# Kernel optimization log

Measured on AMD Instinct MI355X. Metric: run time of the kernel, lower is better.

Reference implementation:

```python
import jax, jax.numpy as jnp
import numpy as np

KS = 3
N_TAPS = KS * KS
PAD = 1
EPS = 1e-5


def conv2d(x, w, b=None, stride=1, padding=1):
    out = jax.lax.conv_general_dilated(
        x, w, (stride, stride), [(padding, padding), (padding, padding)],
        dimension_numbers=('NCHW', 'OIHW', 'NCHW'))
    if b is not None:
        out = out + b[None, :, None, None]
    return out


def deform_conv(x, p_conv_w, p_conv_b, dcn_w):
    # x: (b,c,H,W). Canonical pure-torch DCNv1 (no modulation), stride=1, padding=1.
    off = conv2d(x, p_conv_w, p_conv_b, 1, 1).transpose(0, 2, 3, 1)  # (b,h,w,2N)
    b, h, w, _ = off.shape
    xp = jnp.pad(x, ((0, 0), (0, 0), (PAD, PAD), (PAD, PAD)))  # zero-pad
    Hp, Wp = xp.shape[2], xp.shape[3]
    r = jnp.arange(-(KS - 1) // 2, (KS - 1) // 2 + 1, dtype=x.dtype)
    pn_h, pn_w = [a.reshape(-1) for a in jnp.meshgrid(r, r, indexing='ij')]  # (N,)
    p0_h = jnp.arange(1, h + 1, dtype=x.dtype)[:, None, None]  # (h,1,1)
    p0_w = jnp.arange(1, w + 1, dtype=x.dtype)[None, :, None]  # (1,w,1)
    ph = jnp.clip(p0_h + pn_h + off[..., :N_TAPS], 0, Hp - 1)   # (b,h,w,N)
    pw = jnp.clip(p0_w + pn_w + off[..., N_TAPS:], 0, Wp - 1)
    fh, fw = jnp.floor(ph), jnp.floor(pw)
    lt_h = jnp.clip(fh, 0, Hp - 1); lt_w = jnp.clip(fw, 0, Wp - 1)
    rb_h = jnp.clip(fh + 1, 0, Hp - 1); rb_w = jnp.clip(fw + 1, 0, Wp - 1)
    g_lt = (1 + (lt_h - ph)) * (1 + (lt_w - pw))
    g_rb = (1 - (rb_h - ph)) * (1 - (rb_w - pw))
    g_lb = (1 + (lt_h - ph)) * (1 - (rb_w - pw))
    g_rt = (1 - (rb_h - ph)) * (1 + (lt_w - pw))
    ilt_h, ilt_w = lt_h.astype(jnp.int32), lt_w.astype(jnp.int32)
    irb_h, irb_w = rb_h.astype(jnp.int32), rb_w.astype(jnp.int32)
    gather = jax.vmap(lambda im, iy, ix: im[:, iy, ix])  # per-sample -> (c,h,w,N)
    x_lt = gather(xp, ilt_h, ilt_w)
    x_rb = gather(xp, irb_h, irb_w)
    x_lb = gather(xp, ilt_h, irb_w)
    x_rt = gather(xp, irb_h, ilt_w)
    xo = (g_lt[:, None] * x_lt + g_rb[:, None] * x_rb +
          g_lb[:, None] * x_lb + g_rt[:, None] * x_rt)  # (b,c,h,w,N)
    O, C = dcn_w.shape[0], dcn_w.shape[1]
    # reshape-to-(h*ks,w*ks) + stride-ks conv == contraction over tap n = ky*ks+kx
    return jnp.einsum('bchwn,ocn->bohw', xo, dcn_w.reshape(O, C, N_TAPS))


def batchnorm(x, gamma, beta):
    mu = x.mean((0, 2, 3), keepdims=True)
    var = ((x - mu) ** 2).mean((0, 2, 3), keepdims=True)  # biased var (torch BN)
    return gamma[None, :, None, None] * (x - mu) * jax.lax.rsqrt(var + EPS) + beta[None, :, None, None]


def setup_inputs() -> dict:
    key = jax.random.key(0)
    ks = jax.random.split(key, 8)
    B, C, O, H, W = 8, 64, 128, 128, 128
    return {
        'x': jax.random.normal(ks[0], (B, C, H, W), jnp.float32),
        'p_conv_w': jax.random.normal(ks[1], (2 * N_TAPS, C, 3, 3), jnp.float32) * 0.01,
        'p_conv_b': jax.random.normal(ks[2], (2 * N_TAPS,), jnp.float32) * 0.1,
        'dcn_w': jax.random.normal(ks[3], (C, C, 3, 3), jnp.float32) * 0.05,
        'bn_gamma': jnp.ones((C,), jnp.float32) + 0.1 * jax.random.normal(ks[4], (C,), jnp.float32),
        'bn_beta': 0.1 * jax.random.normal(ks[5], (C,), jnp.float32),
        'conv2_w': jax.random.normal(ks[6], (O, C, 3, 3), jnp.float32) * 0.05,
        'conv2_b': jax.random.normal(ks[7], (O,), jnp.float32) * 0.05,
    }


def reference(x, p_conv_w, p_conv_b, dcn_w, bn_gamma, bn_beta, conv2_w, conv2_b):
    out = deform_conv(x, p_conv_w, p_conv_b, dcn_w)
    out = jax.nn.relu(batchnorm(out, bn_gamma, bn_beta))
    out = out + x
    return conv2d(out, conv2_w, conv2_b, 1, 1)  # (B, 128, 128, 128)
```

## Files before the change

### kernel.cpp

```cpp
#include <hip/hip_runtime.h>
#include <hip/hip_bf16.h>

#define BB 8
#define CC 64
#define OO 128
#define HH 128
#define WW 128
#define HW (HH*WW)
#define NTAP 9

typedef float f32x4 __attribute__((ext_vector_type(4)));
typedef short short8 __attribute__((ext_vector_type(8)));

__device__ __forceinline__ uint f2bf(float v) {
    uint b = __float_as_uint(v);
    return (b + 0x7FFFu + ((b >> 16) & 1u)) >> 16;
}

__device__ __forceinline__ float sampf(const float* __restrict__ xc, int iy, int ix) {
    unsigned uy = (unsigned)(iy - 1), ux = (unsigned)(ix - 1);
    return (uy < 128u && ux < 128u) ? xc[uy * 128 + ux] : 0.f;
}

__global__ void k_repack(const float* __restrict__ pw, const float* __restrict__ dw,
                         const float* __restrict__ cw,
                         float* __restrict__ wp1, float* __restrict__ wpd,
                         ushort* __restrict__ wb2) {
    int i = blockIdx.x * 256 + threadIdx.x;
    if (i < 10368) {
        int o = i % 18, t = (i / 18) % 9, c = i / 162;
        wp1[i] = pw[(o * 64 + c) * 9 + t];
    }
    if (i < 36864) {
        int o = i % 64, t = (i / 64) % 9, c = i / 576;
        wpd[i] = dw[(o * 64 + c) * 9 + t];
    }
    if (i < 73728) {
        int j = i & 7, lane = (i >> 3) & 63, ot = (i >> 9) & 7;
        int kc = (i >> 12) & 1, t = i >> 13;
        int c = kc * 32 + (lane >> 4) * 8 + j;
        int oc = ot * 16 + (lane & 15);
        wb2[i] = (ushort)f2bf(cw[(oc * 64 + c) * 9 + t]);
    }
}

__global__ __launch_bounds__(256) void k_pconv(const float* __restrict__ x,
                                               const float* __restrict__ wp1,
                                               const float* __restrict__ pb,
                                               float* __restrict__ off) {
    int tile = blockIdx.x;
    int b = blockIdx.y;
    int ty0 = (tile / 8) * 16, tx0 = (tile % 8) * 16;
    int tid = threadIdx.x;
    int py = tid / 16, px = tid % 16;
    __shared__ float lx[16][18 * 18];

    float acc[18];
#pragma unroll
    for (int o = 0; o < 18; o++) acc[o] = pb[o];

    for (int cc = 0; cc < 4; cc++) {
        __syncthreads();
        for (int idx = tid; idx < 16 * 324; idx += 256) {
            int c = idx / 324, r = (idx % 324) / 18, col = idx % 18;
            int gy = ty0 + r - 1, gx = tx0 + col - 1;
            float v = 0.f;
            if ((unsigned)gy < 128u && (unsigned)gx < 128u)
                v = x[((b * 64 + cc * 16 + c) * 128 + gy) * 128 + gx];
            lx[c][r * 18 + col] = v;
        }
        __syncthreads();
        for (int c = 0; c < 16; c++) {
#pragma unroll
            for (int t = 0; t < 9; t++) {
                float xv = lx[c][(py + t / 3) * 18 + px + t % 3];
                const float* wr = wp1 + ((cc * 16 + c) * 9 + t) * 18;
#pragma unroll
                for (int o = 0; o < 18; o++) acc[o] = fmaf(xv, wr[o], acc[o]);
            }
        }
    }
    int yy = ty0 + py, xx = tx0 + px;
#pragma unroll
    for (int o = 0; o < 18; o++)
        off[((b * 18 + o) * 128 + yy) * 128 + xx] = acc[o];
}

__global__ __launch_bounds__(256) void k_deform(const float* __restrict__ x,
                                                const float* __restrict__ off,
                                                const float* __restrict__ wpd,
                                                float* __restrict__ y) {
    int tile = blockIdx.x;
    int b = blockIdx.y;
    int ty0 = (tile / 16) * 8, tx0 = (tile % 16) * 8;
    int tid = threadIdx.x;

    __shared__ uint   mwin[576];
    __shared__ float4 mwt[576];
    __shared__ uint   xtile[4 * 256];
    __shared__ uint   xo[4][580];

    for (int e = tid; e < 576; e += 256) {
        int n = e >> 6, p = e & 63;
        int py = p >> 3, px = p & 7;
        int yy = ty0 + py, xx = tx0 + px;
        float offh = off[((b * 18 + n) * 128 + yy) * 128 + xx];
        float offw = off[((b * 18 + 9 + n) * 128 + yy) * 128 + xx];
        float ph = (float)(yy + 1) + (float)(n / 3 - 1) + offh;
        float pw = (float)(xx + 1) + (float)(n % 3 - 1) + offw;
        ph = fminf(fmaxf(ph, 0.f), 129.f);
        pw = fminf(fmaxf(pw, 0.f), 129.f);
        float fh = floorf(ph), fw = floorf(pw);
        int lth = (int)fh, ltw = (int)fw;
        int rbh = min(lth + 1, 129), rbw = min(ltw + 1, 129);
        float dh_l = 1.f + (fh - ph);
        float dh_r = 1.f - ((float)rbh - ph);
        float dw_l = 1.f + (fw - pw);
        float dw_r = 1.f - ((float)rbw - pw);
        int uy0 = lth - 1, ux0 = ltw - 1, uy1 = rbh - 1, ux1 = rbw - 1;
        bool iy0 = (unsigned)uy0 < 128u, ix0 = (unsigned)ux0 < 128u;
        bool iy1 = (unsigned)uy1 < 128u, ix1 = (unsigned)ux1 < 128u;
        float w_lt = (iy0 && ix0) ? dh_l * dw_l : 0.f;
        float w_rb = (iy1 && ix1) ? dh_r * dw_r : 0.f;
        float w_lb = (iy0 && ix1) ? dh_l * dw_r : 0.f;
        float w_rt = (iy1 && ix0) ? dh_r * dw_l : 0.f;
        mwt[e] = make_float4(w_lt, w_rb, w_lb, w_rt);
        int wy0 = uy0 - ty0 + 4, wx0 = ux0 - tx0 + 4;
        int wy1 = uy1 - ty0 + 4, wx1 = ux1 - tx0 + 4;
        uint win = 0xFFFFFFFFu;
        if ((unsigned)wy0 < 16u && (unsigned)wx0 < 16u &&
            (unsigned)wy1 < 16u && (unsigned)wx1 < 16u) {
            uint o00 = (uint)(wy0 * 16 + wx0);
            uint o11 = (uint)(wy1 * 16 + wx1);
            uint o01 = (uint)(wy0 * 16 + wx1);
            uint o10 = (uint)(wy1 * 16 + wx0);
            win = o00 | (o11 << 8) | (o01 << 16) | (o10 << 24);
        }
        mwin[e] = win;
    }

    float acc[16] = {};
    int cg = tid >> 6;
    int l64 = tid & 63;
    int cgoff = cg * 256;
    int ob = __builtin_amdgcn_readfirstlane(cg * 16);

    int sgy = ty0 - 4 + (tid >> 4), sgx = tx0 - 4 + (tid & 15);
    bool sinb = ((unsigned)sgy < 128u && (unsigned)sgx < 128u);
    int spos = sgy * 128 + sgx;

    for (int cc = 0; cc < 8; cc++) {
#pragma unroll
        for (int q = 0; q < 4; q++) {
            int c0 = cc * 8 + 2 * q;
            float v0 = 0.f, v1 = 0.f;
            if (sinb) {
                v0 = x[(size_t)(b * 64 + c0) * HW + spos];
                v1 = x[(size_t)(b * 64 + c0 + 1) * HW + spos];
            }
            xtile[q * 256 + tid] = (f2bf(v1) << 16) | f2bf(v0);
        }
        __syncthreads();
#pragma unroll 2
        for (int i = 0; i < 9; i++) {
            int e = l64 + 64 * i;
            uint w = mwin[e];
            float4 g = mwt[e];
            float vlo, vhi;
            if (__builtin_expect(w != 0xFFFFFFFFu, 1)) {
                uint u00 = xtile[cgoff + (w & 255u)];
                uint u11 = xtile[cgoff + ((w >> 8) & 255u)];
                uint u01 = xtile[cgoff + ((w >> 16) & 255u)];
                uint u10 = xtile[cgoff + (w >> 24)];
                float a00l = __uint_as_float(u00 << 16), a00h = __uint_as_float(u00 & 0xFFFF0000u);
                float a11l = __uint_as_float(u11 << 16), a11h = __uint_as_float(u11 & 0xFFFF0000u);
                float a01l = __uint_as_float(u01 << 16), a01h = __uint_as_float(u01 & 0xFFFF0000u);
                float a10l = __uint_as_float(u10 << 16), a10h = __uint_as_float(u10 & 0xFFFF0000u);
                vlo = g.x * a00l + g.y * a11l + g.z * a01l + g.w * a10l;
                vhi = g.x * a00h + g.y * a11h + g.z * a01h + g.w * a10h;
            } else {
                int n = e >> 6, p = e & 63;
                int yy2 = ty0 + (p >> 3), xx2 = tx0 + (p & 7);
                float offh = off[((b * 18 + n) * 128 + yy2) * 128 + xx2];
                float offw = off[((b * 18 + 9 + n) * 128 + yy2) * 128 + xx2];
                float ph = fminf(fmaxf((float)(yy2 + 1) + (float)(n / 3 - 1) + offh, 0.f), 129.f);
                float pw = fminf(fmaxf((float)(xx2 + 1) + (float)(n % 3 - 1) + offw, 0.f), 129.f);
                int lth = (int)floorf(ph), ltw = (int)floorf(pw);
                int rbh = min(lth + 1, 129), rbw = min(ltw + 1, 129);
                const float* xc0 = x + (size_t)(b * 64 + cc * 8 + 2 * cg) * HW;
                const float* xc1 = xc0 + HW;
                vlo = g.x * sampf(xc0, lth, ltw) + g.y * sampf(xc0, rbh, rbw)
                    + g.z * sampf(xc0, lth, rbw) + g.w * sampf(xc0, rbh, ltw);
                vhi = g.x * sampf(xc1, lth, ltw) + g.y * sampf(xc1, rbh, rbw)
                    + g.z * sampf(xc1, lth, rbw) + g.w * sampf(xc1, rbh, ltw);
            }
            xo[cg][e] = (f2bf(vhi) << 16) | f2bf(vlo);
        }
        __syncthreads();
        for (int q = 0; q < 4; q++) {
#pragma unroll
            for (int n = 0; n < 9; n++) {
                uint u = xo[q][n * 64 + l64];
                float xlo = __uint_as_float(u << 16);
                float xhi = __uint_as_float(u & 0xFFFF0000u);
                const float* w0 = wpd + (((cc * 8 + 2 * q) * 9 + n) * 64) + ob;
                const float* w1 = w0 + 576;
#pragma unroll
                for (int j = 0; j < 16; j++) acc[j] = fmaf(xlo, w0[j], acc[j]);
#pragma unroll
                for (int j = 0; j < 16; j++) acc[j] = fmaf(xhi, w1[j], acc[j]);
            }
        }
        __syncthreads();
    }

    int yy = ty0 + (l64 >> 3), xx = tx0 + (l64 & 7);
#pragma unroll
    for (int j = 0; j < 16; j++)
        y[(size_t)(b * 64 + ob + j) * HW + yy * 128 + xx] = acc[j];
}

__global__ __launch_bounds__(256) void k_bnpart(const float* __restrict__ y,
                                                float* __restrict__ part) {
    int c = blockIdx.x, b = blockIdx.y;
    int tid = threadIdx.x;
    const float4* p = (const float4*)(y + (size_t)(b * 64 + c) * HW);
    float s = 0.f, sq = 0.f;
    for (int i = tid; i < HW / 4; i += 256) {
        float4 v = p[i];
        s += v.x + v.y + v.z + v.w;
        sq += v.x * v.x + v.y * v.y + v.z * v.z + v.w * v.w;
    }
#pragma unroll
    for (int o = 32; o > 0; o >>= 1) {
        s += __shfl_down(s, o);
        sq += __shfl_down(sq, o);
    }
    __shared__ float rs[4], rq[4];
    int wid = tid >> 6;
    if ((tid & 63) == 0) { rs[wid] = s; rq[wid] = sq; }
    __syncthreads();
    if (tid == 0) {
        part[(b * 64 + c) * 2]     = rs[0] + rs[1] + rs[2] + rs[3];
        part[(b * 64 + c) * 2 + 1] = rq[0] + rq[1] + rq[2] + rq[3];
    }
}

__global__ void k_bnfinal(const float* __restrict__ part,
                          const float* __restrict__ gamma,
                          const float* __restrict__ beta,
                          float* __restrict__ ss) {
    int c = threadIdx.x;
    float s = 0.f, sq = 0.f;
#pragma unroll
    for (int b = 0; b < 8; b++) {
        s += part[(b * 64 + c) * 2];
        sq += part[(b * 64 + c) * 2 + 1];
    }
    const float inv = 1.f / (float)(8 * HW);
    float mean = s * inv;
    float var = sq * inv - mean * mean;
    float scale = gamma[c] * rsqrtf(var + 1e-5f);
    ss[c] = scale;
    ss[64 + c] = beta[c] - mean * scale;
}

__global__ __launch_bounds__(256) void k_conv2(const float* __restrict__ x,
                                               const float* __restrict__ y,
                                               const float* __restrict__ ss,
                                               const ushort* __restrict__ wb2,
                                               const float* __restrict__ b2,
                                               float* __restrict__ out) {
    int tile = blockIdx.x, b = blockIdx.y;
    int ty0 = (tile / 16) * 8, tx0 = (tile % 16) * 8;
    int tid = threadIdx.x;

    __shared__ uint lz[3600];

    for (int idx = tid; idx < 3200; idx += 256) {
        int q = idx / 100, pos = idx % 100;
        int r = pos / 10, col = pos % 10;
        int gy = ty0 + r - 1, gx = tx0 + col - 1;
        uint u = 0;
        if ((unsigned)gy < 128u && (unsigned)gx < 128u) {
            int c0 = q * 2;
            int gi = ((b * 64 + c0) * HW) + gy * 128 + gx;
            float t0 = fmaf(y[gi], ss[c0], ss[64 + c0]);
            float v0 = fmaxf(t0, 0.f) + x[gi];
            float t1 = fmaf(y[gi + HW], ss[c0 + 1], ss[65 + c0]);
            float v1 = fmaxf(t1, 0.f) + x[gi + HW];
            u = (f2bf(v1) << 16) | f2bf(v0);
        }
        lz[pos * 36 + q] = u;
    }
    __syncthreads();

    int lane = tid & 63, pg = tid >> 6;
    int r16 = lane & 15, jg = lane >> 4;
    int p = pg * 16 + r16;
    int pyA = p >> 3, pxA = p & 7;

    f32x4 acc[8];
#pragma unroll
    for (int ot = 0; ot < 8; ot++) {
        float bv = b2[ot * 16 + r16];
        acc[ot] = (f32x4){bv, bv, bv, bv};
    }

#pragma unroll
    for (int t = 0; t < 9; t++) {
        int pos = (pyA + t / 3) * 10 + (pxA + t % 3);
#pragma unroll
        for (int kc = 0; kc < 2; kc++) {
            short8 av = *(const short8*)(lz + pos * 36 + kc * 16 + jg * 4);
            const ushort* wk = wb2 + (t * 2 + kc) * 4096 + lane * 8;
#pragma unroll
            for (int ot = 0; ot < 8; ot++) {
                short8 bv = *(const short8*)(wk + ot * 512);
                acc[ot] = __builtin_amdgcn_mfma_f32_16x16x32_bf16(av, bv, acc[ot], 0, 0, 0);
            }
        }
    }

    int p0 = pg * 16 + jg * 4;
    int yy = ty0 + (p0 >> 3), xx = tx0 + (p0 & 7);
#pragma unroll
    for (int ot = 0; ot < 8; ot++) {
        int oc = ot * 16 + r16;
        *(f32x4*)(out + (size_t)(b * 128 + oc) * HW + yy * 128 + xx) = acc[ot];
    }
}

extern "C" void kernel_launch(void* const* d_in, const int* in_sizes, int n_in,
                              void* d_out, int out_size, void* d_ws, size_t ws_size,
                              hipStream_t stream) {
    const float* x     = (const float*)d_in[0];
    const float* pw    = (const float*)d_in[1];
    const float* pb    = (const float*)d_in[2];
    const float* dw    = (const float*)d_in[3];
    const float* gamma = (const float*)d_in[4];
    const float* beta  = (const float*)d_in[5];
    const float* cw    = (const float*)d_in[6];
    const float* cb    = (const float*)d_in[7];
    float* out = (float*)d_out;
    float* ws  = (float*)d_ws;

    float*  wp1  = ws;
    float*  ss   = ws + 10368;
    float*  part = ws + 10496;
    float*  wpd  = ws + 11520;
    ushort* wb2  = (ushort*)(ws + 48384);
    float*  off  = ws + 85248;
    float*  yb   = ws + 2444544;

    k_repack<<<dim3(288), dim3(256), 0, stream>>>(pw, dw, cw, wp1, wpd, wb2);
    k_pconv<<<dim3(64, 8), dim3(256), 0, stream>>>(x, wp1, pb, off);
    k_deform<<<dim3(256, 8), dim3(256), 0, stream>>>(x, off, wpd, yb);
    k_bnpart<<<dim3(64, 8), dim3(256), 0, stream>>>(yb, part);
    k_bnfinal<<<dim3(1), dim3(64), 0, stream>>>(part, gamma, beta, ss);
    k_conv2<<<dim3(256, 8), dim3(256), 0, stream>>>(x, yb, ss, wb2, cb, out);
}
```

Before: 350.5 us.

## Split offset conv channels across half-blocks with shared-memory reduction and smaller tiles

The offset-predicting conv now uses 16x8 output tiles, with the two halves of each block covering different input-channel halves, and their partial sums are combined through shared memory. This doubles the grid to 1024 blocks so the GPU is filled better and each thread runs a shorter serial chain of FMAs. The cost is a larger halo fraction when loading tiles, an extra shared-memory reduction and barrier, and half the threads sitting idle during the final store.

```diff
diff --git a/kernel.cpp b/kernel.cpp
--- a/kernel.cpp
+++ b/kernel.cpp
@@ -50,40 +50,53 @@
                                                float* __restrict__ off) {
     int tile = blockIdx.x;
     int b = blockIdx.y;
-    int ty0 = (tile / 8) * 16, tx0 = (tile % 8) * 16;
+    int ty0 = (tile >> 3) * 8, tx0 = (tile & 7) * 16;
     int tid = threadIdx.x;
-    int py = tid / 16, px = tid % 16;
-    __shared__ float lx[16][18 * 18];
+    int px = tid & 127;
+    int ch = tid >> 7;
+    int pyr = px >> 4, pxl = px & 15;
+
+    __shared__ float lx[32][180];
+    __shared__ float pacc[128][19];
 
     float acc[18];
 #pragma unroll
-    for (int o = 0; o < 18; o++) acc[o] = pb[o];
-
-    for (int cc = 0; cc < 4; cc++) {
-        __syncthreads();
-        for (int idx = tid; idx < 16 * 324; idx += 256) {
-            int c = idx / 324, r = (idx % 324) / 18, col = idx % 18;
+    for (int o = 0; o < 18; o++) acc[o] = 0.f;
+
+    for (int h = 0; h < 2; h++) {
+        __syncthreads();
+        for (int idx = tid; idx < 5760; idx += 256) {
+            int c = idx / 180, pos = idx % 180;
+            int r = pos / 18, col = pos % 18;
             int gy = ty0 + r - 1, gx = tx0 + col - 1;
             float v = 0.f;
             if ((unsigned)gy < 128u && (unsigned)gx < 128u)
-                v = x[((b * 64 + cc * 16 + c) * 128 + gy) * 128 + gx];
-            lx[c][r * 18 + col] = v;
-        }
-        __syncthreads();
-        for (int c = 0; c < 16; c++) {
+                v = x[((b * 64 + h * 32 + c) * 128 + gy) * 128 + gx];
+            lx[c][pos] = v;
+        }
+        __syncthreads();
+        for (int ci = 0; ci < 16; ci++) {
+            int c = ch * 16 + ci;
 #pragma unroll
             for (int t = 0; t < 9; t++) {
-                float xv = lx[c][(py + t / 3) * 18 + px + t % 3];
-                const float* wr = wp1 + ((cc * 16 + c) * 9 + t) * 18;
+                float xv = lx[c][(pyr + t / 3) * 18 + pxl + t % 3];
+                const float* wr = wp1 + ((h * 32 + c) * 9 + t) * 18;
 #pragma unroll
                 for (int o = 0; o < 18; o++) acc[o] = fmaf(xv, wr[o], acc[o]);
             }
         }
     }
-    int yy = ty0 + py, xx = tx0 + px;
-#pragma unroll
-    for (int o = 0; o < 18; o++)
-        off[((b * 18 + o) * 128 + yy) * 128 + xx] = acc[o];
+    if (ch == 1) {
+#pragma unroll
+        for (int o = 0; o < 18; o++) pacc[px][o] = acc[o];
+    }
+    __syncthreads();
+    if (ch == 0) {
+        int yy = ty0 + pyr, xx = tx0 + pxl;
+#pragma unroll
+        for (int o = 0; o < 18; o++)
+            off[((b * 18 + o) * 128 + yy) * 128 + xx] = acc[o] + pacc[px][o] + pb[o];
+    }
 }
 
 __global__ __launch_bounds__(256) void k_deform(const float* __restrict__ x,
@@ -354,7 +367,7 @@
     float*  yb   = ws + 2444544;
 
     k_repack<<<dim3(288), dim3(256), 0, stream>>>(pw, dw, cw, wp1, wpd, wb2);
-    k_pconv<<<dim3(64, 8), dim3(256), 0, stream>>>(x, wp1, pb, off);
+    k_pconv<<<dim3(128, 8), dim3(256), 0, stream>>>(x, wp1, pb, off);
     k_deform<<<dim3(256, 8), dim3(256), 0, stream>>>(x, off, wpd, yb);
     k_bnpart<<<dim3(64, 8), dim3(256), 0, stream>>>(yb, part);
     k_bnfinal<<<dim3(1), dim3(64), 0, stream>>>(part, gamma, beta, ss);
```

Result: slower. 439.0 us (+25.2%).
